# Kernel tuning notes

Hardware: AMD Instinct MI355X
Metric: run time of the kernel (lower is better)

Reference implementation:

```python
import itertools
import jax, jax.numpy as jnp
import numpy as np

NUM_GROUPS = 2  # num_squeeze_group
LN_EPS = 1e-6


def setup_inputs() -> dict:
    key = jax.random.key(0)
    ks = jax.random.split(key, 8)
    B, F, D = 1024, 32, 64
    P = F * (F - 1) // 2  # 496 pairs
    OUT = 512
    g = NUM_GROUPS
    red = max(1, F * g * 2 // 4)  # reduction_ratio = 4 -> 32
    emb_size = F * D
    return {
        "x": jax.random.normal(ks[0], (B, F, D), jnp.float32),
        "W1": jax.random.normal(ks[1], (F * 2 * g, red), jnp.float32) * (1.0 / np.sqrt(F * 2 * g)),
        "b1": jnp.zeros((red,), jnp.float32),
        "W2": jax.random.normal(ks[2], (red, emb_size), jnp.float32) * (1.0 / np.sqrt(red)),
        "b2": jnp.zeros((emb_size,), jnp.float32),
        "ln_scale": jnp.ones((emb_size,), jnp.float32),
        "ln_bias": jnp.zeros((emb_size,), jnp.float32),
        "Wp": jax.random.normal(ks[3], (P, D, D), jnp.float32) * (1.0 / np.sqrt(D)),
        "bp": jnp.zeros((P, D), jnp.float32),
        "Wo": jax.random.normal(ks[4], (P, OUT), jnp.float32) * (1.0 / np.sqrt(P)),
        "bo": jnp.zeros((OUT,), jnp.float32),
    }


def _pair_indices(F):
    pairs = np.array(list(itertools.combinations(range(F), 2)), dtype=np.int32)
    return pairs[:, 0], pairs[:, 1]


def reference(x, W1, b1, W2, b2, ln_scale, ln_bias, Wp, bp, Wo, bo):
    B, F, D = x.shape
    g = NUM_GROUPS

    # ---- SENet ----
    xg = x.reshape(B, F, g, D // g)
    # per-field [max(g), mean(g)], concatenated over fields -> [B, F*2g]
    z = jnp.concatenate([xg.max(axis=-1), xg.mean(axis=-1)], axis=-1).reshape(B, F * 2 * g)
    a1 = jax.nn.relu(z @ W1 + b1)            # [B, red]
    weights = a1 @ W2 + b2                   # [B, F*D]
    flat = x.reshape(B, F * D)
    senet = flat * weights + flat            # skip connection
    # layer norm over last axis
    mu = senet.mean(axis=-1, keepdims=True)
    var = senet.var(axis=-1, keepdims=True)
    senet = (senet - mu) * jax.lax.rsqrt(var + LN_EPS) * ln_scale + ln_bias

    # ---- BiLinear ('interaction', use_plus=True) ----
    i_idx, j_idx = _pair_indices(F)
    xi = x[:, i_idx, :]                      # [B, P, D]
    xj = x[:, j_idx, :]                      # [B, P, D]
    proj = jnp.einsum('bpd,pde->bpe', xi, Wp) + bp  # per-pair Dense(D->D)
    dots = jnp.sum(proj * xj, axis=-1)       # [B, P] batched dot (bi-linear+)
    bilinear = dots @ Wo + bo                # [B, OUT]

    return jnp.concatenate([senet, bilinear], axis=-1)
```

## Files before the change

### kernel.cpp

```cpp
#include <hip/hip_runtime.h>
#include <hip/hip_bf16.h>

#define F_FEAT 32
#define D_DIM 64
#define B_SZ 1024
#define EMB 2048
#define P_PAIRS 496
#define KPAD 512
#define OUT_N 512
#define OUT_STRIDE 2560
#define LN_EPS 1e-6f

typedef __attribute__((ext_vector_type(8))) short bf16x8;
typedef __attribute__((ext_vector_type(4))) float f32x4;

__device__ inline ushort f2bf(float f) {
    union { float f; unsigned u; } a; a.f = f;
    unsigned u = a.u;
    unsigned r = (u + 0x7FFFu + ((u >> 16) & 1u)) >> 16;
    return (ushort)r;
}

__global__ __launch_bounds__(256) void k_prep(
        const float* __restrict__ x, ushort* __restrict__ xb,
        const float* __restrict__ Wp, ushort* __restrict__ Wpt,
        const float* __restrict__ Wo, ushort* __restrict__ Wot,
        ushort* __restrict__ db) {
    __shared__ float tile[64][65];
    int t = threadIdx.x;
    int blk = blockIdx.x;

    if (blk < 1024) {
        size_t base = ((size_t)blk * 256 + t) * 8;
        float4 v0 = *reinterpret_cast<const float4*>(x + base);
        float4 v1 = *reinterpret_cast<const float4*>(x + base + 4);
        bf16x8 o;
        o[0] = f2bf(v0.x); o[1] = f2bf(v0.y); o[2] = f2bf(v0.z); o[3] = f2bf(v0.w);
        o[4] = f2bf(v1.x); o[5] = f2bf(v1.y); o[6] = f2bf(v1.z); o[7] = f2bf(v1.w);
        *reinterpret_cast<bf16x8*>(xb + base) = o;
    } else if (blk < 1520) {
        int p = blk - 1024;
        const float* src = Wp + (size_t)p * 4096;
        ushort* dst = Wpt + (size_t)p * 4096;
#pragma unroll
        for (int it = 0; it < 4; ++it) {
            int d = it * 16 + (t >> 4);
            int e4 = (t & 15) * 4;
            float4 v = *reinterpret_cast<const float4*>(src + d * 64 + e4);
            tile[d][e4] = v.x; tile[d][e4 + 1] = v.y; tile[d][e4 + 2] = v.z; tile[d][e4 + 3] = v.w;
        }
        __syncthreads();
#pragma unroll
        for (int it = 0; it < 4; ++it) {
            int e = it * 16 + (t >> 4);
            int d4 = (t & 15) * 4;
            ushort4 o;
            o.x = f2bf(tile[d4][e]);     o.y = f2bf(tile[d4 + 1][e]);
            o.z = f2bf(tile[d4 + 2][e]); o.w = f2bf(tile[d4 + 3][e]);
            *reinterpret_cast<ushort4*>(dst + e * 64 + d4) = o;
        }
    } else if (blk < 1584) {
        int bidx = blk - 1520;
        int k0 = (bidx & 7) * 64;
        int n0 = (bidx >> 3) * 64;
#pragma unroll
        for (int it = 0; it < 4; ++it) {
            int kr = it * 16 + (t >> 4);
            int nc = (t & 15) * 4;
            int k = k0 + kr;
            float4 v = {0.f, 0.f, 0.f, 0.f};
            if (k < P_PAIRS) v = *reinterpret_cast<const float4*>(Wo + (size_t)k * OUT_N + n0 + nc);
            tile[kr][nc] = v.x; tile[kr][nc + 1] = v.y; tile[kr][nc + 2] = v.z; tile[kr][nc + 3] = v.w;
        }
        __syncthreads();
#pragma unroll
        for (int it = 0; it < 4; ++it) {
            int nr = it * 16 + (t >> 4);
            int kc = (t & 15) * 4;
            ushort4 o;
            o.x = f2bf(tile[kc][nr]);     o.y = f2bf(tile[kc + 1][nr]);
            o.z = f2bf(tile[kc + 2][nr]); o.w = f2bf(tile[kc + 3][nr]);
            *reinterpret_cast<ushort4*>(Wot + (size_t)(n0 + nr) * KPAD + k0 + kc) = o;
        }
    } else {
        int tid = (blk - 1584) * 256 + t;
        if (tid < B_SZ) {
            bf16x8 z = {0, 0, 0, 0, 0, 0, 0, 0};
            ushort* dstp = db + (size_t)tid * KPAD + P_PAIRS;
            *reinterpret_cast<bf16x8*>(dstp) = z;
            *reinterpret_cast<bf16x8*>(dstp + 8) = z;
        }
    }
}

__global__ __launch_bounds__(512) void k_senet(
        const float* __restrict__ x,
        const float* __restrict__ W1, const float* __restrict__ b1,
        const float* __restrict__ W2, const float* __restrict__ b2,
        const float* __restrict__ ln_s, const float* __restrict__ ln_b,
        float* __restrict__ out) {
    __shared__ float xs[4][EMB];
    __shared__ float zs[4][128];
    __shared__ float a1s[4][32];
    __shared__ float red[2][4][8];
    int t = threadIdx.x;
    int b0 = blockIdx.x * 4;

    for (int r = 0; r < 4; ++r) {
        const float4* src = reinterpret_cast<const float4*>(x + (size_t)(b0 + r) * EMB);
        float4* dstv = reinterpret_cast<float4*>(&xs[r][0]);
        dstv[t] = src[t];
    }
    __syncthreads();

    if (t < 256) {
        int r = t >> 6, f = (t >> 1) & 31, gg = t & 1;
        const float* base = &xs[r][f * 64 + gg * 32];
        float mx = -INFINITY, sm = 0.f;
        for (int q = 0; q < 32; ++q) {
            float v = base[(q + t) & 31];
            mx = fmaxf(mx, v); sm += v;
        }
        zs[r][f * 4 + gg]     = mx;
        zs[r][f * 4 + 2 + gg] = sm * (1.f / 32.f);
    }
    __syncthreads();

    if (t < 128) {
        int r = t >> 5, c = t & 31;
        float acc = b1[c];
        for (int k = 0; k < 128; ++k) acc += zs[r][k] * W1[k * 32 + c];
        a1s[r][c] = fmaxf(acc, 0.f);
    }
    __syncthreads();

    float acc[4][4];
#pragma unroll
    for (int r = 0; r < 4; ++r)
#pragma unroll
        for (int u = 0; u < 4; ++u) acc[r][u] = 0.f;

    for (int k = 0; k < 32; ++k) {
        float a0 = a1s[0][k], a1v = a1s[1][k], a2 = a1s[2][k], a3 = a1s[3][k];
#pragma unroll
        for (int u = 0; u < 4; ++u) {
            float wv = W2[k * EMB + t + 512 * u];
            acc[0][u] += a0 * wv; acc[1][u] += a1v * wv;
            acc[2][u] += a2 * wv; acc[3][u] += a3 * wv;
        }
    }
    float ssum[4], ssq[4];
#pragma unroll
    for (int r = 0; r < 4; ++r) { ssum[r] = 0.f; ssq[r] = 0.f; }
#pragma unroll
    for (int r = 0; r < 4; ++r) {
#pragma unroll
        for (int u = 0; u < 4; ++u) {
            int e = t + 512 * u;
            float w = acc[r][u] + b2[e];
            float s = xs[r][e] * (w + 1.0f);
            xs[r][e] = s;
            ssum[r] += s; ssq[r] += s * s;
        }
    }
    int lane = t & 63, w = t >> 6;
#pragma unroll
    for (int r = 0; r < 4; ++r) {
        float a = ssum[r], q = ssq[r];
        for (int off = 32; off; off >>= 1) { a += __shfl_down(a, off); q += __shfl_down(q, off); }
        if (lane == 0) { red[0][r][w] = a; red[1][r][w] = q; }
    }
    __syncthreads();
    float mu[4], rs[4];
#pragma unroll
    for (int r = 0; r < 4; ++r) {
        float a = 0.f, q = 0.f;
#pragma unroll
        for (int i = 0; i < 8; ++i) { a += red[0][r][i]; q += red[1][r][i]; }
        mu[r] = a * (1.f / 2048.f);
        float var = q * (1.f / 2048.f) - mu[r] * mu[r];
        rs[r] = rsqrtf(var + LN_EPS);
    }
#pragma unroll
    for (int r = 0; r < 4; ++r) {
#pragma unroll
        for (int u = 0; u < 4; ++u) {
            int e = t + 512 * u;
            float s = xs[r][e];
            out[(size_t)(b0 + r) * OUT_STRIDE + e] = (s - mu[r]) * rs[r] * ln_s[e] + ln_b[e];
        }
    }
}

__global__ __launch_bounds__(256) void k_dots(
        const ushort* __restrict__ xb, const ushort* __restrict__ Wpt,
        const float* __restrict__ x, const float* __restrict__ bp,
        ushort* __restrict__ db) {
    int p = blockIdx.x >> 2;
    int q = blockIdx.x & 3;
    int i = 0, rem = p;
    while (rem >= F_FEAT - 1 - i) { rem -= F_FEAT - 1 - i; ++i; }
    int j = i + 1 + rem;

    int wave = threadIdx.x >> 6, lane = threadIdx.x & 63;
    int row = lane & 15, kg = lane >> 4;

    bf16x8 wfr[4][2];
#pragma unroll
    for (int nt = 0; nt < 4; ++nt)
#pragma unroll
        for (int ks = 0; ks < 2; ++ks)
            wfr[nt][ks] = *reinterpret_cast<const bf16x8*>(
                Wpt + (size_t)p * 4096 + (nt * 16 + row) * 64 + ks * 32 + kg * 8);

    f32x4 bb[4];
#pragma unroll
    for (int nt = 0; nt < 4; ++nt)
        bb[nt] = *reinterpret_cast<const f32x4*>(bp + p * 64 + nt * 16 + kg * 4);

#pragma unroll
    for (int it = 0; it < 4; ++it) {
        int b0 = q * 256 + (wave * 4 + it) * 16;

        bf16x8 xifr[2];
#pragma unroll
        for (int ks = 0; ks < 2; ++ks)
            xifr[ks] = *reinterpret_cast<const bf16x8*>(
                xb + (size_t)(b0 + row) * EMB + i * 64 + ks * 32 + kg * 8);

        f32x4 xjv[4];
#pragma unroll
        for (int nt = 0; nt < 4; ++nt)
            xjv[nt] = *reinterpret_cast<const f32x4*>(
                x + (size_t)(b0 + row) * EMB + j * 64 + nt * 16 + kg * 4);

        f32x4 acc[4];
#pragma unroll
        for (int nt = 0; nt < 4; ++nt) {
            f32x4 z = {0.f, 0.f, 0.f, 0.f};
            acc[nt] = z;
            acc[nt] = __builtin_amdgcn_mfma_f32_16x16x32_bf16(wfr[nt][0], xifr[0], acc[nt], 0, 0, 0);
            acc[nt] = __builtin_amdgcn_mfma_f32_16x16x32_bf16(wfr[nt][1], xifr[1], acc[nt], 0, 0, 0);
        }

        float v = 0.f;
#pragma unroll
        for (int nt = 0; nt < 4; ++nt)
#pragma unroll
            for (int r = 0; r < 4; ++r)
                v += (acc[nt][r] + bb[nt][r]) * xjv[nt][r];
        v += __shfl_xor(v, 16);
        v += __shfl_xor(v, 32);
        if (lane < 16)
            db[(size_t)(b0 + lane) * KPAD + p] = f2bf(v);
    }
}

__global__ __launch_bounds__(256) void k_bilin2(
        const ushort* __restrict__ db, const ushort* __restrict__ Wot,
        const float* __restrict__ bo, float* __restrict__ out) {
    int mt  = blockIdx.x >> 4;
    int nt0 = blockIdx.x & 15;
    int wave = threadIdx.x >> 6, lane = threadIdx.x & 63;
    int row = lane & 15, kg = lane >> 4;
    int m0 = mt * 64 + wave * 16;
    int n0 = nt0 * 32;

    f32x4 acc0 = {0.f, 0.f, 0.f, 0.f};
    f32x4 acc1 = {0.f, 0.f, 0.f, 0.f};
    const ushort* arow  = db  + (size_t)(m0 + row) * KPAD + kg * 8;
    const ushort* brow0 = Wot + (size_t)(n0 + row) * KPAD + kg * 8;
    const ushort* brow1 = brow0 + 16 * KPAD;
#pragma unroll
    for (int ks = 0; ks < 16; ++ks) {
        bf16x8 a  = *reinterpret_cast<const bf16x8*>(arow  + ks * 32);
        bf16x8 b0 = *reinterpret_cast<const bf16x8*>(brow0 + ks * 32);
        bf16x8 b1 = *reinterpret_cast<const bf16x8*>(brow1 + ks * 32);
        acc0 = __builtin_amdgcn_mfma_f32_16x16x32_bf16(a, b0, acc0, 0, 0, 0);
        acc1 = __builtin_amdgcn_mfma_f32_16x16x32_bf16(a, b1, acc1, 0, 0, 0);
    }
    int col = row;
    float bo0 = bo[n0 + col], bo1 = bo[n0 + 16 + col];
#pragma unroll
    for (int r = 0; r < 4; ++r) {
        size_t orow = (size_t)(m0 + kg * 4 + r) * OUT_STRIDE + 2048 + n0;
        out[orow + col]      = acc0[r] + bo0;
        out[orow + 16 + col] = acc1[r] + bo1;
    }
}

extern "C" void kernel_launch(void* const* d_in, const int* in_sizes, int n_in,
                              void* d_out, int out_size, void* d_ws, size_t ws_size,
                              hipStream_t stream) {
    const float* x    = (const float*)d_in[0];
    const float* W1   = (const float*)d_in[1];
    const float* b1   = (const float*)d_in[2];
    const float* W2   = (const float*)d_in[3];
    const float* b2   = (const float*)d_in[4];
    const float* ln_s = (const float*)d_in[5];
    const float* ln_b = (const float*)d_in[6];
    const float* Wp   = (const float*)d_in[7];
    const float* bp   = (const float*)d_in[8];
    const float* Wo   = (const float*)d_in[9];
    const float* bo   = (const float*)d_in[10];
    float* out = (float*)d_out;

    ushort* xb   = (ushort*)d_ws;
    ushort* wpt  = (ushort*)((char*)d_ws + 4194304);
    ushort* db   = (ushort*)((char*)d_ws + 4194304 + 4063232);
    ushort* wot  = (ushort*)((char*)d_ws + 4194304 + 4063232 + 1048576);

    k_prep<<<1592, 256, 0, stream>>>(x, xb, Wp, wpt, Wo, wot, db);
    k_senet<<<B_SZ / 4, 512, 0, stream>>>(x, W1, b1, W2, b2, ln_s, ln_b, out);
    k_dots<<<P_PAIRS * 4, 256, 0, stream>>>(xb, wpt, x, bp, db);
    k_bilin2<<<256, 256, 0, stream>>>(db, wot, bo, out);
}
```

Baseline: 62.70 us.

## Fuse x bf16 conversion into SENet and read bf16 x_j in dots kernel

The x-to-bf16 conversion moves out of the prep kernel and into the SENet kernel, which already loads x, so x is read from global memory once less. The dots kernel now reads the x_j operand from the bf16 copy instead of fp32, halving that traffic at the cost of rounding x_j. The dots grid is also halved, with each block covering 512 batch rows in 8 iterations, so the per-pair weight fragments are reused over more rows. This leaves fewer blocks and more serial work per block.

```diff
diff --git a/kernel.cpp b/kernel.cpp
--- a/kernel.cpp
+++ b/kernel.cpp
@@ -20,9 +20,12 @@
     unsigned r = (u + 0x7FFFu + ((u >> 16) & 1u)) >> 16;
     return (ushort)r;
 }
+__device__ inline float bf2f(ushort u) {
+    union { unsigned u; float f; } a; a.u = ((unsigned)u) << 16;
+    return a.f;
+}
 
 __global__ __launch_bounds__(256) void k_prep(
-        const float* __restrict__ x, ushort* __restrict__ xb,
         const float* __restrict__ Wp, ushort* __restrict__ Wpt,
         const float* __restrict__ Wo, ushort* __restrict__ Wot,
         ushort* __restrict__ db) {
@@ -30,16 +33,8 @@
     int t = threadIdx.x;
     int blk = blockIdx.x;
 
-    if (blk < 1024) {
-        size_t base = ((size_t)blk * 256 + t) * 8;
-        float4 v0 = *reinterpret_cast<const float4*>(x + base);
-        float4 v1 = *reinterpret_cast<const float4*>(x + base + 4);
-        bf16x8 o;
-        o[0] = f2bf(v0.x); o[1] = f2bf(v0.y); o[2] = f2bf(v0.z); o[3] = f2bf(v0.w);
-        o[4] = f2bf(v1.x); o[5] = f2bf(v1.y); o[6] = f2bf(v1.z); o[7] = f2bf(v1.w);
-        *reinterpret_cast<bf16x8*>(xb + base) = o;
-    } else if (blk < 1520) {
-        int p = blk - 1024;
+    if (blk < 496) {
+        int p = blk;
         const float* src = Wp + (size_t)p * 4096;
         ushort* dst = Wpt + (size_t)p * 4096;
 #pragma unroll
@@ -59,8 +54,8 @@
             o.z = f2bf(tile[d4 + 2][e]); o.w = f2bf(tile[d4 + 3][e]);
             *reinterpret_cast<ushort4*>(dst + e * 64 + d4) = o;
         }
-    } else if (blk < 1584) {
-        int bidx = blk - 1520;
+    } else if (blk < 560) {
+        int bidx = blk - 496;
         int k0 = (bidx & 7) * 64;
         int n0 = (bidx >> 3) * 64;
 #pragma unroll
@@ -83,7 +78,7 @@
             *reinterpret_cast<ushort4*>(Wot + (size_t)(n0 + nr) * KPAD + k0 + kc) = o;
         }
     } else {
-        int tid = (blk - 1584) * 256 + t;
+        int tid = (blk - 560) * 256 + t;
         if (tid < B_SZ) {
             bf16x8 z = {0, 0, 0, 0, 0, 0, 0, 0};
             ushort* dstp = db + (size_t)tid * KPAD + P_PAIRS;
@@ -94,7 +89,7 @@
 }
 
 __global__ __launch_bounds__(512) void k_senet(
-        const float* __restrict__ x,
+        const float* __restrict__ x, ushort* __restrict__ xb,
         const float* __restrict__ W1, const float* __restrict__ b1,
         const float* __restrict__ W2, const float* __restrict__ b2,
         const float* __restrict__ ln_s, const float* __restrict__ ln_b,
@@ -108,8 +103,11 @@
 
     for (int r = 0; r < 4; ++r) {
         const float4* src = reinterpret_cast<const float4*>(x + (size_t)(b0 + r) * EMB);
-        float4* dstv = reinterpret_cast<float4*>(&xs[r][0]);
-        dstv[t] = src[t];
+        float4 v = src[t];
+        reinterpret_cast<float4*>(&xs[r][0])[t] = v;
+        ushort4 o;
+        o.x = f2bf(v.x); o.y = f2bf(v.y); o.z = f2bf(v.z); o.w = f2bf(v.w);
+        *reinterpret_cast<ushort4*>(xb + (size_t)(b0 + r) * EMB + t * 4) = o;
     }
     __syncthreads();
 
@@ -194,10 +192,9 @@
 
 __global__ __launch_bounds__(256) void k_dots(
         const ushort* __restrict__ xb, const ushort* __restrict__ Wpt,
-        const float* __restrict__ x, const float* __restrict__ bp,
-        ushort* __restrict__ db) {
-    int p = blockIdx.x >> 2;
-    int q = blockIdx.x & 3;
+        const float* __restrict__ bp, ushort* __restrict__ db) {
+    int p = blockIdx.x >> 1;
+    int h = blockIdx.x & 1;
     int i = 0, rem = p;
     while (rem >= F_FEAT - 1 - i) { rem -= F_FEAT - 1 - i; ++i; }
     int j = i + 1 + rem;
@@ -219,8 +216,8 @@
         bb[nt] = *reinterpret_cast<const f32x4*>(bp + p * 64 + nt * 16 + kg * 4);
 
 #pragma unroll
-    for (int it = 0; it < 4; ++it) {
-        int b0 = q * 256 + (wave * 4 + it) * 16;
+    for (int it = 0; it < 8; ++it) {
+        int b0 = h * 512 + (wave * 8 + it) * 16;
 
         bf16x8 xifr[2];
 #pragma unroll
@@ -228,11 +225,11 @@
             xifr[ks] = *reinterpret_cast<const bf16x8*>(
                 xb + (size_t)(b0 + row) * EMB + i * 64 + ks * 32 + kg * 8);
 
-        f32x4 xjv[4];
+        ushort4 xjw[4];
 #pragma unroll
         for (int nt = 0; nt < 4; ++nt)
-            xjv[nt] = *reinterpret_cast<const f32x4*>(
-                x + (size_t)(b0 + row) * EMB + j * 64 + nt * 16 + kg * 4);
+            xjw[nt] = *reinterpret_cast<const ushort4*>(
+                xb + (size_t)(b0 + row) * EMB + j * 64 + nt * 16 + kg * 4);
 
         f32x4 acc[4];
 #pragma unroll
@@ -245,10 +242,12 @@
 
         float v = 0.f;
 #pragma unroll
-        for (int nt = 0; nt < 4; ++nt)
-#pragma unroll
-            for (int r = 0; r < 4; ++r)
-                v += (acc[nt][r] + bb[nt][r]) * xjv[nt][r];
+        for (int nt = 0; nt < 4; ++nt) {
+            v += (acc[nt][0] + bb[nt][0]) * bf2f(xjw[nt].x);
+            v += (acc[nt][1] + bb[nt][1]) * bf2f(xjw[nt].y);
+            v += (acc[nt][2] + bb[nt][2]) * bf2f(xjw[nt].z);
+            v += (acc[nt][3] + bb[nt][3]) * bf2f(xjw[nt].w);
+        }
         v += __shfl_xor(v, 16);
         v += __shfl_xor(v, 32);
         if (lane < 16)
@@ -310,8 +309,8 @@
     ushort* db   = (ushort*)((char*)d_ws + 4194304 + 4063232);
     ushort* wot  = (ushort*)((char*)d_ws + 4194304 + 4063232 + 1048576);
 
-    k_prep<<<1592, 256, 0, stream>>>(x, xb, Wp, wpt, Wo, wot, db);
-    k_senet<<<B_SZ / 4, 512, 0, stream>>>(x, W1, b1, W2, b2, ln_s, ln_b, out);
-    k_dots<<<P_PAIRS * 4, 256, 0, stream>>>(xb, wpt, x, bp, db);
+    k_prep<<<568, 256, 0, stream>>>(Wp, wpt, Wo, wot, db);
+    k_senet<<<B_SZ / 4, 512, 0, stream>>>(x, xb, W1, b1, W2, b2, ln_s, ln_b, out);
+    k_dots<<<P_PAIRS * 2, 256, 0, stream>>>(xb, wpt, bp, db);
     k_bilin2<<<256, 256, 0, stream>>>(db, wot, bo, out);
 }
```

New measurement: 59.18 us. 5.6% less time.
